# Kernel tuning notes

Hardware: AMD Instinct MI355X
Metric: run time of the kernel (lower is better)

The kernel has to match this reference:

```python
import jax, jax.numpy as jnp
import numpy as np

DIM = 128
HEADS = 4
EPS = 1e-5


def setup_inputs() -> dict:
    key = jax.random.key(0)
    ks = jax.random.split(key, 14)
    B, N, C = 1, 256, DIM
    s = 1.0 / np.sqrt(C)
    inp = {
        'pair': jax.random.normal(ks[0], (B, N, N, C), dtype=jnp.float32),
        'Wq': jax.random.normal(ks[1], (C, C), dtype=jnp.float32) * s,
        'bq': jnp.zeros((C,), dtype=jnp.float32),
        'Wk': jax.random.normal(ks[2], (C, C), dtype=jnp.float32) * s,
        'bk': jnp.zeros((C,), dtype=jnp.float32),
        'Wv': jax.random.normal(ks[3], (C, C), dtype=jnp.float32) * s,
        'bv': jnp.zeros((C,), dtype=jnp.float32),
        'Wg': jax.random.normal(ks[4], (C, C), dtype=jnp.float32) * s,
        'bg': jnp.zeros((C,), dtype=jnp.float32),
        'Wo': jax.random.normal(ks[5], (C, C), dtype=jnp.float32) * s,
        'bo': jnp.zeros((C,), dtype=jnp.float32),
        'gamma': jnp.ones((C,), dtype=jnp.float32),
        'beta': jnp.zeros((C,), dtype=jnp.float32),
    }
    return inp


def _layernorm(x, gamma, beta):
    mu = jnp.mean(x, axis=-1, keepdims=True)
    var = jnp.mean(jnp.square(x - mu), axis=-1, keepdims=True)
    return (x - mu) * jax.lax.rsqrt(var + EPS) * gamma + beta


def reference(pair, Wq, bq, Wk, bk, Wv, bv, Wg, bg, Wo, bo, gamma, beta):
    B, N, _, C = pair.shape
    H = HEADS
    Ch = C // H
    scale = Ch ** (-0.5)
    # projections: nn.Linear is x @ W.T + b
    q = (pair @ Wq.T + bq).reshape(B, N, N, H, Ch)
    k = (pair @ Wk.T + bk).reshape(B, N, N, H, Ch)
    v = (pair @ Wv.T + bv).reshape(B, N, N, H, Ch)
    # per-row attention: logits [B,H,N(i),N(j),N(k)]
    attn = jnp.einsum('bijhc,bikhc->bhijk', q, k) * scale
    attn = jax.nn.softmax(attn, axis=-1)
    out = jnp.einsum('bhijk,bikhc->bijhc', attn, v).reshape(B, N, N, C)
    gate = jax.nn.sigmoid(pair @ Wg.T + bg)
    out = out * gate
    out = out @ Wo.T + bo
    return _layernorm(pair + out, gamma, beta)
```

## Files before the change

### kernel.cpp

```cpp
#include <hip/hip_runtime.h>
#include <hip/hip_bf16.h>

#define NN 256
#define CC 128

typedef __attribute__((ext_vector_type(8))) short bf16x8;
typedef __attribute__((ext_vector_type(4))) short bf16x4;
typedef __attribute__((ext_vector_type(4))) float f32x4;

static __device__ __forceinline__ short f2bf(float f) {
  union { float f; unsigned u; } un; un.f = f;
  unsigned r = un.u + 0x7fff + ((un.u >> 16) & 1);
  return (short)(r >> 16);
}
static __device__ __forceinline__ float bf2f(short s) {
  union { unsigned u; float f; } un;
  un.u = ((unsigned)(unsigned short)s) << 16;
  return un.f;
}

__global__ void prep_kernel(const float* __restrict__ Wq, const float* __restrict__ Wk,
                            const float* __restrict__ Wv, const float* __restrict__ Wg,
                            const float* __restrict__ Wo, short* __restrict__ wpk)
{
  const int c = blockIdx.x * 256 + threadIdx.x;
  const int w = c >> 11;
  const int rem = c & 2047;
  const int nt = rem >> 8;
  const int kc = (rem >> 6) & 3;
  const int lane = rem & 63;
  const float* W = (w == 0) ? Wq : (w == 1) ? Wk : (w == 2) ? Wv : (w == 3) ? Wg : Wo;
  const int row = nt * 16 + (lane & 15);
  const int col = kc * 32 + (lane >> 4) * 8;
  const float* src = W + row * CC + col;
  bf16x8 b;
  #pragma unroll
  for (int j = 0; j < 8; ++j) b[j] = f2bf(src[j]);
  *(bf16x8*)(wpk + (size_t)c * 8) = b;
}

__global__ __launch_bounds__(256, 2) void proj_kernel(
    const float* __restrict__ pair, const short* __restrict__ wpk,
    const float* __restrict__ bq, const float* __restrict__ bk,
    const float* __restrict__ bv, const float* __restrict__ bg,
    short* __restrict__ qo, short* __restrict__ ko,
    short* __restrict__ vo, short* __restrict__ go)
{
  const int wid  = threadIdx.x >> 6;
  const int lane = threadIdx.x & 63;
  const int g    = lane >> 4;
  const int t16  = lane & 15;

  const short* wsrc = wpk + (size_t)wid * 16384;
  bf16x8 wf[8][4];
  #pragma unroll
  for (int nt = 0; nt < 8; ++nt)
    #pragma unroll
    for (int kc = 0; kc < 4; ++kc)
      wf[nt][kc] = *(const bf16x8*)(wsrc + ((nt*4 + kc)*64 + lane)*8);

  const float* bias = (wid == 0) ? bq : (wid == 1) ? bk : (wid == 2) ? bv : bg;
  f32x4 bcol[8];
  #pragma unroll
  for (int nt = 0; nt < 8; ++nt) bcol[nt] = *(const f32x4*)(bias + nt*16 + g*4);

  short* outp = (wid == 0) ? qo : (wid == 1) ? ko : (wid == 2) ? vo : go;
  const int row0 = blockIdx.x * 64;

  f32x4 rawA[8];
  {
    const float* p0 = pair + (size_t)(row0 + t16) * CC + g*8;
    #pragma unroll
    for (int kc = 0; kc < 4; ++kc) {
      rawA[kc*2]     = *(const f32x4*)(p0 + kc*32);
      rawA[kc*2 + 1] = *(const f32x4*)(p0 + kc*32 + 4);
    }
  }

  #pragma unroll
  for (int mc = 0; mc < 4; ++mc) {
    const int m = row0 + mc*16 + t16;
    f32x4 rawB[8];
    if (mc < 3) {
      const float* pn = pair + (size_t)(m + 16) * CC + g*8;
      #pragma unroll
      for (int kc = 0; kc < 4; ++kc) {
        rawB[kc*2]     = *(const f32x4*)(pn + kc*32);
        rawB[kc*2 + 1] = *(const f32x4*)(pn + kc*32 + 4);
      }
    }

    bf16x8 pf[4];
    #pragma unroll
    for (int kc = 0; kc < 4; ++kc) {
      bf16x8 a;
      #pragma unroll
      for (int j = 0; j < 8; ++j) a[j] = f2bf(rawA[kc*2 + (j>>2)][j&3]);
      pf[kc] = a;
    }

    f32x4 acc[8];
    #pragma unroll
    for (int nt = 0; nt < 8; ++nt) acc[nt] = f32x4{0.f,0.f,0.f,0.f};
    #pragma unroll
    for (int kc = 0; kc < 4; ++kc)
      #pragma unroll
      for (int nt = 0; nt < 8; ++nt)
        acc[nt] = __builtin_amdgcn_mfma_f32_16x16x32_bf16(wf[nt][kc], pf[kc], acc[nt], 0, 0, 0);

    const size_t rowoff = (size_t)m * CC;
    #pragma unroll
    for (int nt = 0; nt < 8; ++nt) {
      f32x4 v;
      #pragma unroll
      for (int r = 0; r < 4; ++r) v[r] = acc[nt][r] + bcol[nt][r];
      if (wid == 3) {
        #pragma unroll
        for (int r = 0; r < 4; ++r) v[r] = 1.f / (1.f + __expf(-v[r]));
      }
      bf16x4 pk;
      #pragma unroll
      for (int r = 0; r < 4; ++r) pk[r] = f2bf(v[r]);
      *(bf16x4*)(outp + rowoff + nt*16 + g*4) = pk;
    }

    if (mc < 3) {
      #pragma unroll
      for (int u = 0; u < 8; ++u) rawA[u] = rawB[u];
    }
  }
}

__global__ __launch_bounds__(256) void attn_kernel(
    const short* __restrict__ qi, const short* __restrict__ ki,
    const short* __restrict__ vi, short* __restrict__ ao)
{
  __shared__ short Vsl[32*256];
  __shared__ short Pl[4][2048];

  const int bid  = blockIdx.x;
  const int i    = bid >> 2, h = bid & 3;
  const int tid  = threadIdx.x;
  const int wid  = tid >> 6, lane = tid & 63;
  const int g    = lane >> 4, t16 = lane & 15;
  const size_t mbase = (size_t)i * NN;

  {
    const short* vr = vi + (mbase + tid) * CC + h*32;
    #pragma unroll
    for (int u = 0; u < 4; ++u) {
      bf16x8 v8 = *(const bf16x8*)(vr + u*8);
      #pragma unroll
      for (int e = 0; e < 8; ++e) {
        const int ch = u*8 + e;
        Vsl[ch*256 + (tid ^ ((ch & 7) << 3))] = v8[e];
      }
    }
  }
  __syncthreads();

  const float cs = 0.17677669529663689f * 1.4426950408889634f;
  const int swzP = (t16 & 7) << 3;
  const int ch0 = t16, ch1 = 16 + t16;
  const int swzV0 = (ch0 & 7) << 3, swzV1 = (ch1 & 7) << 3;
  short* Pw = &Pl[wid][0];

  #pragma unroll 1
  for (int cc = 0; cc < 4; ++cc) {
    const int q0 = wid*64 + cc*16;
    bf16x8 qf = *(const bf16x8*)(qi + (mbase + q0 + t16)*CC + h*32 + g*8);

    f32x4 s[16];
    #pragma unroll
    for (int t = 0; t < 16; ++t) {
      bf16x8 kf = *(const bf16x8*)(ki + (mbase + t*16 + t16)*CC + h*32 + g*8);
      s[t] = __builtin_amdgcn_mfma_f32_16x16x32_bf16(kf, qf, f32x4{0.f,0.f,0.f,0.f}, 0, 0, 0);
    }

    f32x4 m4 = s[0];
    #pragma unroll
    for (int t = 1; t < 16; ++t)
      #pragma unroll
      for (int r = 0; r < 4; ++r) m4[r] = fmaxf(m4[r], s[t][r]);
    float mx = fmaxf(fmaxf(m4[0], m4[1]), fmaxf(m4[2], m4[3]));
    mx = fmaxf(mx, __shfl_xor(mx, 16));
    mx = fmaxf(mx, __shfl_xor(mx, 32));

    f32x4 s4 = f32x4{0.f,0.f,0.f,0.f};
    #pragma unroll
    for (int t = 0; t < 16; ++t) {
      f32x4 v = s[t];
      #pragma unroll
      for (int r = 0; r < 4; ++r) { v[r] = exp2f((v[r] - mx) * cs); s4[r] += v[r]; }
      s[t] = v;
    }
    float sum = (s4[0] + s4[1]) + (s4[2] + s4[3]);
    sum += __shfl_xor(sum, 16);
    sum += __shfl_xor(sum, 32);
    const float sm = 1.f / sum;

    f32x4 o0 = f32x4{0.f,0.f,0.f,0.f};
    f32x4 o1 = f32x4{0.f,0.f,0.f,0.f};
    #pragma unroll
    for (int half = 0; half < 2; ++half) {
      asm volatile("s_waitcnt lgkmcnt(0)" ::: "memory");
      #pragma unroll
      for (int tt = 0; tt < 8; ++tt) {
        const int t = half*8 + tt;
        bf16x4 pk;
        #pragma unroll
        for (int r = 0; r < 4; ++r) pk[r] = f2bf(s[t][r]);
        *(bf16x4*)&Pw[t16*128 + ((tt*16 + g*4) ^ swzP)] = pk;
      }
      asm volatile("s_waitcnt lgkmcnt(0)" ::: "memory");

      bf16x8 pa[4];
      #pragma unroll
      for (int kc = 0; kc < 4; ++kc)
        pa[kc] = *(const bf16x8*)&Pw[t16*128 + ((kc*32 + g*8) ^ swzP)];

      #pragma unroll
      for (int kc = 0; kc < 4; ++kc) {
        const int kb = half*128 + kc*32 + g*8;
        bf16x8 v0 = *(const bf16x8*)&Vsl[ch0*256 + (kb ^ swzV0)];
        bf16x8 v1 = *(const bf16x8*)&Vsl[ch1*256 + (kb ^ swzV1)];
        o0 = __builtin_amdgcn_mfma_f32_16x16x32_bf16(v0, pa[kc], o0, 0, 0, 0);
        o1 = __builtin_amdgcn_mfma_f32_16x16x32_bf16(v1, pa[kc], o1, 0, 0, 0);
      }
    }

    const size_t ob = (mbase + q0 + t16)*CC + h*32;
    bf16x4 pk0, pk1;
    #pragma unroll
    for (int r = 0; r < 4; ++r) { pk0[r] = f2bf(o0[r] * sm); pk1[r] = f2bf(o1[r] * sm); }
    *(bf16x4*)(ao + ob + g*4)      = pk0;
    *(bf16x4*)(ao + ob + 16 + g*4) = pk1;
  }
}

__global__ __launch_bounds__(256) void out_kernel(
    const short* __restrict__ ai, const short* __restrict__ gi,
    const short* __restrict__ wpk_o, const float* __restrict__ bo,
    const float* __restrict__ pair, const float* __restrict__ gamma,
    const float* __restrict__ beta, float* __restrict__ out)
{
  __shared__ short Wl[16384];
  const int tid = threadIdx.x;
  const int wid = tid >> 6, lane = tid & 63;
  const int g = lane >> 4, t16 = lane & 15;

  const int m0 = blockIdx.x*64 + wid*16;
  const size_t rowoff = (size_t)(m0 + t16) * CC;

  bf16x8 a8[4], g8[4];
  #pragma unroll
  for (int kc = 0; kc < 4; ++kc) {
    a8[kc] = *(const bf16x8*)(ai + rowoff + kc*32 + g*8);
    g8[kc] = *(const bf16x8*)(gi + rowoff + kc*32 + g*8);
  }

  #pragma unroll
  for (int it = 0; it < 8; ++it) {
    const int c = it*256 + tid;
    *(bf16x8*)&Wl[c*8] = *(const bf16x8*)(wpk_o + (size_t)c*8);
  }
  __syncthreads();

  bf16x8 xf[4];
  #pragma unroll
  for (int kc = 0; kc < 4; ++kc) {
    bf16x8 o;
    #pragma unroll
    for (int j = 0; j < 8; ++j) o[j] = f2bf(bf2f(a8[kc][j]) * bf2f(g8[kc][j]));
    xf[kc] = o;
  }

  f32x4 acc[8];
  #pragma unroll
  for (int nt = 0; nt < 8; ++nt) acc[nt] = f32x4{0.f,0.f,0.f,0.f};
  #pragma unroll
  for (int kc = 0; kc < 4; ++kc)
    #pragma unroll
    for (int nt = 0; nt < 8; ++nt) {
      bf16x8 wfr = *(const bf16x8*)&Wl[((nt*4 + kc)*64 + lane)*8];
      acc[nt] = __builtin_amdgcn_mfma_f32_16x16x32_bf16(wfr, xf[kc], acc[nt], 0, 0, 0);
    }

  float val[8][4];
  #pragma unroll
  for (int nt = 0; nt < 8; ++nt) {
    f32x4 b4 = *(const f32x4*)(bo + nt*16 + g*4);
    f32x4 p4 = *(const f32x4*)(pair + rowoff + nt*16 + g*4);
    #pragma unroll
    for (int r = 0; r < 4; ++r) val[nt][r] = acc[nt][r] + b4[r] + p4[r];
  }
  float sum = 0.f;
  #pragma unroll
  for (int nt = 0; nt < 8; ++nt)
    #pragma unroll
    for (int r = 0; r < 4; ++r) sum += val[nt][r];
  sum += __shfl_xor(sum, 16); sum += __shfl_xor(sum, 32);
  const float mu = sum * (1.f/128.f);
  float sq = 0.f;
  #pragma unroll
  for (int nt = 0; nt < 8; ++nt)
    #pragma unroll
    for (int r = 0; r < 4; ++r) { float d = val[nt][r] - mu; sq += d*d; }
  sq += __shfl_xor(sq, 16); sq += __shfl_xor(sq, 32);
  const float rstd = rsqrtf(sq * (1.f/128.f) + 1e-5f);

  #pragma unroll
  for (int nt = 0; nt < 8; ++nt) {
    f32x4 g4 = *(const f32x4*)(gamma + nt*16 + g*4);
    f32x4 b4 = *(const f32x4*)(beta  + nt*16 + g*4);
    f32x4 o4;
    #pragma unroll
    for (int r = 0; r < 4; ++r) o4[r] = (val[nt][r] - mu) * rstd * g4[r] + b4[r];
    *(f32x4*)(out + rowoff + nt*16 + g*4) = o4;
  }
}

extern "C" void kernel_launch(void* const* d_in, const int* in_sizes, int n_in,
                              void* d_out, int out_size, void* d_ws, size_t ws_size,
                              hipStream_t stream) {
  const float* pair  = (const float*)d_in[0];
  const float* Wq    = (const float*)d_in[1];
  const float* bq    = (const float*)d_in[2];
  const float* Wk    = (const float*)d_in[3];
  const float* bk    = (const float*)d_in[4];
  const float* Wv    = (const float*)d_in[5];
  const float* bv    = (const float*)d_in[6];
  const float* Wg    = (const float*)d_in[7];
  const float* bg    = (const float*)d_in[8];
  const float* Wo    = (const float*)d_in[9];
  const float* bo    = (const float*)d_in[10];
  const float* gamma = (const float*)d_in[11];
  const float* beta  = (const float*)d_in[12];
  float* out = (float*)d_out;

  short* wpk  = (short*)d_ws;
  short* q_ws = wpk + 81920;
  short* k_ws = q_ws + 8388608;
  short* v_ws = k_ws + 8388608;
  short* g_ws = v_ws + 8388608;
  short* a_ws = q_ws;

  hipLaunchKernelGGL(prep_kernel, dim3(40), dim3(256), 0, stream,
                     Wq, Wk, Wv, Wg, Wo, wpk);
  hipLaunchKernelGGL(proj_kernel, dim3(1024), dim3(256), 0, stream,
                     pair, wpk, bq, bk, bv, bg, q_ws, k_ws, v_ws, g_ws);
  hipLaunchKernelGGL(attn_kernel, dim3(1024), dim3(256), 0, stream,
                     q_ws, k_ws, v_ws, a_ws);
  hipLaunchKernelGGL(out_kernel, dim3(1024), dim3(256), 0, stream,
                     a_ws, g_ws, wpk + 4*16384, bo, pair, gamma, beta, out);
}
```

Baseline: 198.4 us.

## Split projection per block with LDS weights, halve attention query work per block

The projection kernel now gives each block a single projection, staged once in shared memory, and spreads 256 rows across four waves, instead of each wave holding its own weight set in registers. This frees registers and lifts the occupancy cap. The attention grid doubles so each block handles half the query rows, which raises parallelism but loads each V slice into shared memory twice. The explicit LDS waitcnt barriers are dropped, and out_kernel issues its residual pair loads early to hide their latency. The trade-off is more repeated reads of pair and V across blocks.

Result: slower. 218.6 us (+10.2%).

```diff
diff --git a/kernel.cpp b/kernel.cpp
--- a/kernel.cpp
+++ b/kernel.cpp
@@ -39,33 +39,36 @@
   *(bf16x8*)(wpk + (size_t)c * 8) = b;
 }
 
-__global__ __launch_bounds__(256, 2) void proj_kernel(
+__global__ __launch_bounds__(256) void proj_kernel(
     const float* __restrict__ pair, const short* __restrict__ wpk,
     const float* __restrict__ bq, const float* __restrict__ bk,
     const float* __restrict__ bv, const float* __restrict__ bg,
     short* __restrict__ qo, short* __restrict__ ko,
     short* __restrict__ vo, short* __restrict__ go)
 {
-  const int wid  = threadIdx.x >> 6;
-  const int lane = threadIdx.x & 63;
+  __shared__ short Wl[16384];
+  const int tid  = threadIdx.x;
+  const int wid  = tid >> 6;
+  const int lane = tid & 63;
   const int g    = lane >> 4;
   const int t16  = lane & 15;
 
-  const short* wsrc = wpk + (size_t)wid * 16384;
-  bf16x8 wf[8][4];
-  #pragma unroll
-  for (int nt = 0; nt < 8; ++nt)
-    #pragma unroll
-    for (int kc = 0; kc < 4; ++kc)
-      wf[nt][kc] = *(const bf16x8*)(wsrc + ((nt*4 + kc)*64 + lane)*8);
-
-  const float* bias = (wid == 0) ? bq : (wid == 1) ? bk : (wid == 2) ? bv : bg;
+  const int pj = blockIdx.x & 3;
+  const int ib = blockIdx.x >> 2;
+
+  #pragma unroll
+  for (int it = 0; it < 8; ++it) {
+    const int c = it*256 + tid;
+    *(bf16x8*)&Wl[c*8] = *(const bf16x8*)(wpk + (size_t)pj*16384 + (size_t)c*8);
+  }
+
+  const float* bias = (pj == 0) ? bq : (pj == 1) ? bk : (pj == 2) ? bv : bg;
   f32x4 bcol[8];
   #pragma unroll
   for (int nt = 0; nt < 8; ++nt) bcol[nt] = *(const f32x4*)(bias + nt*16 + g*4);
-
-  short* outp = (wid == 0) ? qo : (wid == 1) ? ko : (wid == 2) ? vo : go;
-  const int row0 = blockIdx.x * 64;
+  short* outp = (pj == 0) ? qo : (pj == 1) ? ko : (pj == 2) ? vo : go;
+
+  const int row0 = ib*256 + wid*64;
 
   f32x4 rawA[8];
   {
@@ -76,6 +79,7 @@
       rawA[kc*2 + 1] = *(const f32x4*)(p0 + kc*32 + 4);
     }
   }
+  __syncthreads();
 
   #pragma unroll
   for (int mc = 0; mc < 4; ++mc) {
@@ -105,8 +109,10 @@
     #pragma unroll
     for (int kc = 0; kc < 4; ++kc)
       #pragma unroll
-      for (int nt = 0; nt < 8; ++nt)
-        acc[nt] = __builtin_amdgcn_mfma_f32_16x16x32_bf16(wf[nt][kc], pf[kc], acc[nt], 0, 0, 0);
+      for (int nt = 0; nt < 8; ++nt) {
+        bf16x8 wfr = *(const bf16x8*)&Wl[((nt*4 + kc)*64 + lane)*8];
+        acc[nt] = __builtin_amdgcn_mfma_f32_16x16x32_bf16(wfr, pf[kc], acc[nt], 0, 0, 0);
+      }
 
     const size_t rowoff = (size_t)m * CC;
     #pragma unroll
@@ -114,7 +120,7 @@
       f32x4 v;
       #pragma unroll
       for (int r = 0; r < 4; ++r) v[r] = acc[nt][r] + bcol[nt][r];
-      if (wid == 3) {
+      if (pj == 3) {
         #pragma unroll
         for (int r = 0; r < 4; ++r) v[r] = 1.f / (1.f + __expf(-v[r]));
       }
@@ -139,7 +145,9 @@
   __shared__ short Pl[4][2048];
 
   const int bid  = blockIdx.x;
-  const int i    = bid >> 2, h = bid & 3;
+  const int qh2  = bid & 1;
+  const int h    = (bid >> 1) & 3;
+  const int i    = bid >> 3;
   const int tid  = threadIdx.x;
   const int wid  = tid >> 6, lane = tid & 63;
   const int g    = lane >> 4, t16 = lane & 15;
@@ -166,8 +174,8 @@
   short* Pw = &Pl[wid][0];
 
   #pragma unroll 1
-  for (int cc = 0; cc < 4; ++cc) {
-    const int q0 = wid*64 + cc*16;
+  for (int cc = 0; cc < 2; ++cc) {
+    const int q0 = qh2*128 + wid*32 + cc*16;
     bf16x8 qf = *(const bf16x8*)(qi + (mbase + q0 + t16)*CC + h*32 + g*8);
 
     f32x4 s[16];
@@ -203,7 +211,6 @@
     f32x4 o1 = f32x4{0.f,0.f,0.f,0.f};
     #pragma unroll
     for (int half = 0; half < 2; ++half) {
-      asm volatile("s_waitcnt lgkmcnt(0)" ::: "memory");
       #pragma unroll
       for (int tt = 0; tt < 8; ++tt) {
         const int t = half*8 + tt;
@@ -212,7 +219,6 @@
         for (int r = 0; r < 4; ++r) pk[r] = f2bf(s[t][r]);
         *(bf16x4*)&Pw[t16*128 + ((tt*16 + g*4) ^ swzP)] = pk;
       }
-      asm volatile("s_waitcnt lgkmcnt(0)" ::: "memory");
 
       bf16x8 pa[4];
       #pragma unroll
@@ -258,6 +264,10 @@
     a8[kc] = *(const bf16x8*)(ai + rowoff + kc*32 + g*8);
     g8[kc] = *(const bf16x8*)(gi + rowoff + kc*32 + g*8);
   }
+  f32x4 p4[8];
+  #pragma unroll
+  for (int nt = 0; nt < 8; ++nt)
+    p4[nt] = *(const f32x4*)(pair + rowoff + nt*16 + g*4);
 
   #pragma unroll
   for (int it = 0; it < 8; ++it) {
@@ -290,9 +300,8 @@
   #pragma unroll
   for (int nt = 0; nt < 8; ++nt) {
     f32x4 b4 = *(const f32x4*)(bo + nt*16 + g*4);
-    f32x4 p4 = *(const f32x4*)(pair + rowoff + nt*16 + g*4);
-    #pragma unroll
-    for (int r = 0; r < 4; ++r) val[nt][r] = acc[nt][r] + b4[r] + p4[r];
+    #pragma unroll
+    for (int r = 0; r < 4; ++r) val[nt][r] = acc[nt][r] + b4[r] + p4[nt][r];
   }
   float sum = 0.f;
   #pragma unroll
@@ -349,7 +358,7 @@
                      Wq, Wk, Wv, Wg, Wo, wpk);
   hipLaunchKernelGGL(proj_kernel, dim3(1024), dim3(256), 0, stream,
                      pair, wpk, bq, bk, bv, bg, q_ws, k_ws, v_ws, g_ws);
-  hipLaunchKernelGGL(attn_kernel, dim3(1024), dim3(256), 0, stream,
+  hipLaunchKernelGGL(attn_kernel, dim3(2048), dim3(256), 0, stream,
                      q_ws, k_ws, v_ws, a_ws);
   hipLaunchKernelGGL(out_kernel, dim3(1024), dim3(256), 0, stream,
                      a_ws, g_ws, wpk + 4*16384, bo, pair, gamma, beta, out);
```
